# Optimization experiments

Measured on AMD Instinct MI355X. Metric: run time of the kernel, lower is better.

Reference implementation:

```python
import jax, jax.numpy as jnp
import numpy as np
import math

B, L, D, H = 4, 4096, 1024, 16
DH = D // H  # 64


def setup_inputs() -> dict:
    key = jax.random.key(0)
    ks = jax.random.split(key, 11)
    s = 1.0 / math.sqrt(D)
    return {
        "query": jax.random.normal(ks[0], (B, L, D), jnp.float32),
        "key_": jax.random.normal(ks[1], (B, L, D), jnp.float32),
        "value": jax.random.normal(ks[2], (B, L, D), jnp.float32),
        "Wq": jax.random.normal(ks[3], (D, D), jnp.float32) * s,
        "bq": jax.random.normal(ks[4], (D,), jnp.float32) * s,
        "Wk": jax.random.normal(ks[5], (D, D), jnp.float32) * s,
        "bk": jax.random.normal(ks[6], (D,), jnp.float32) * s,
        "Wv": jax.random.normal(ks[7], (D, D), jnp.float32) * s,
        "bv": jax.random.normal(ks[8], (D,), jnp.float32) * s,
        "Wo": jax.random.normal(ks[9], (D, D), jnp.float32) * s,
        "bo": jax.random.normal(ks[10], (D,), jnp.float32) * s,
    }


def reference(query, key_, value, Wq, bq, Wk, bk, Wv, bv, Wo, bo):
    # Linear projections (torch Linear: x @ W.T + b)
    q = (query @ Wq.T + bq).reshape(B, L, DH, H)   # heads in LAST dim (faithful quirk)
    k = (key_ @ Wk.T + bk).reshape(B, L, DH, H)
    v = (value @ Wv.T + bv).reshape(B, L, DH, H)
    # per-(batch, position) matmul: [B,L,DH,H] @ [B,L,H,DH] -> [B,L,DH,DH]
    scores = jnp.einsum('blih,bljh->blij', q, k) * jnp.asarray(math.sqrt(D), q.dtype)
    attn = jax.nn.softmax(scores, axis=-1)
    out = jnp.einsum('blij,bljh->blih', attn, v).reshape(B, L, D)
    return out @ Wo.T + bo
```

## Files before the change

### kernel.cpp

```cpp
#include <hip/hip_runtime.h>

typedef float    f32x4 __attribute__((ext_vector_type(4)));
typedef _Float16 h16x8 __attribute__((ext_vector_type(8)));
typedef _Float16 h16x4 __attribute__((ext_vector_type(4)));

#define DEV __device__ __forceinline__

DEV void async_load16(const void* g, void* l) {
  __builtin_amdgcn_global_load_lds((const __attribute__((address_space(1))) void*)g,
                                   (__attribute__((address_space(3))) void*)l,
                                   16, 0, 0);
}

template <bool OF32>
DEV void gemm256_core(const _Float16* __restrict__ A, const _Float16* __restrict__ Bw,
                      const float* __restrict__ bias, void* Cv, int bm, int bn) {
  constexpr int N = 1024;
  __shared__ __align__(16) _Float16 lds[2 * 2 * 2 * 8192];
  char* ldsb = (char*)lds;

  const int tid  = threadIdx.x;
  const int lane = tid & 63;
  const int w    = tid >> 6;
  const int wm   = w >> 2, wn = w & 3;
  const int m16  = lane & 15, q = lane >> 4;
  const int rowbase = bm << 8;
  const int colbase = bn << 8;

  const int sr0 = (w * 2 + 0) * 16 + (lane >> 2);
  const int sr1 = (w * 2 + 1) * 16 + (lane >> 2);
  const int ss  = lane & 3;
  const int sc0 = ((ss ^ ((sr0 ^ (sr0 >> 2)) & 3)) * 8);
  const int sc1 = ((ss ^ ((sr1 ^ (sr1 >> 2)) & 3)) * 8);

  auto stA = [&](int buf, int kk, int gk) {
    async_load16(A + (size_t)(rowbase + sr0) * 1024 + gk + kk * 32 + sc0,
                 ldsb + buf * 65536 + kk * 16384 + (w * 2 + 0) * 1024);
    async_load16(A + (size_t)(rowbase + sr1) * 1024 + gk + kk * 32 + sc1,
                 ldsb + buf * 65536 + kk * 16384 + (w * 2 + 1) * 1024);
  };
  auto stB = [&](int buf, int kk, int gk) {
    async_load16(Bw + (size_t)(colbase + sr0) * 1024 + gk + kk * 32 + sc0,
                 ldsb + buf * 65536 + 32768 + kk * 16384 + (w * 2 + 0) * 1024);
    async_load16(Bw + (size_t)(colbase + sr1) * 1024 + gk + kk * 32 + sc1,
                 ldsb + buf * 65536 + 32768 + kk * 16384 + (w * 2 + 1) * 1024);
  };

  int aoff[8], boff[4];
#pragma unroll
  for (int mt = 0; mt < 8; ++mt) {
    const int r = wm * 128 + mt * 16 + m16;
    aoff[mt] = r * 64 + ((q ^ ((r ^ (r >> 2)) & 3)) * 16);
  }
#pragma unroll
  for (int nt = 0; nt < 4; ++nt) {
    const int r = wn * 64 + nt * 16 + m16;
    boff[nt] = r * 64 + ((q ^ ((r ^ (r >> 2)) & 3)) * 16);
  }

  f32x4 acc[8][4];
#pragma unroll
  for (int nt = 0; nt < 4; ++nt) {
    const float bv = bias[colbase + wn * 64 + nt * 16 + m16];
#pragma unroll
    for (int mt = 0; mt < 8; ++mt) acc[mt][nt] = {bv, bv, bv, bv};
  }

  stA(0, 0, 0); stB(0, 0, 0); stA(0, 1, 0); stB(0, 1, 0);
  stA(1, 0, 64); stB(1, 0, 64);
  asm volatile("s_waitcnt vmcnt(4)" ::: "memory");
  __builtin_amdgcn_s_barrier();
  __builtin_amdgcn_sched_barrier(0);

  h16x8 bfr[4];

#define PHASE(BUF_, KK_, MH_, STAGE_, VM_)                                      \
  {                                                                             \
    const char* pA = ldsb + (BUF_) * 65536 + (KK_) * 16384;                     \
    const char* pB = pA + 32768;                                                \
    h16x8 a[4];                                                                 \
    _Pragma("unroll")                                                           \
    for (int m_ = 0; m_ < 4; ++m_)                                              \
      a[m_] = *(const h16x8*)(pA + aoff[(MH_) * 4 + m_]);                       \
    if ((MH_) == 0) {                                                           \
      _Pragma("unroll")                                                         \
      for (int n_ = 0; n_ < 4; ++n_)                                            \
        bfr[n_] = *(const h16x8*)(pB + boff[n_]);                               \
    }                                                                           \
    STAGE_                                                                      \
    VM_                                                                         \
    __builtin_amdgcn_s_barrier();                                               \
    asm volatile("s_waitcnt lgkmcnt(0)" ::: "memory");                          \
    __builtin_amdgcn_sched_barrier(0);                                          \
    __builtin_amdgcn_s_setprio(1);                                              \
    _Pragma("unroll")                                                           \
    for (int m_ = 0; m_ < 4; ++m_)                                              \
      _Pragma("unroll")                                                         \
      for (int n_ = 0; n_ < 4; ++n_)                                            \
        acc[(MH_) * 4 + m_][n_] = __builtin_amdgcn_mfma_f32_16x16x32_f16(       \
            a[m_], bfr[n_], acc[(MH_) * 4 + m_][n_], 0, 0, 0);                  \
    __builtin_amdgcn_s_setprio(0);                                              \
    __builtin_amdgcn_s_barrier();                                               \
    __builtin_amdgcn_sched_barrier(0);                                          \
  }

  for (int i = 0; i < 7; ++i) {
    const int g1 = (2 * i + 1) * 64, g2 = (2 * i + 2) * 64, g3 = (2 * i + 3) * 64;
    PHASE(0, 0, 0, { stA(1, 1, g1); stB(1, 1, g1); }, {})
    PHASE(0, 0, 1, {}, {})
    PHASE(0, 1, 0, { stA(0, 0, g2); }, {})
    PHASE(0, 1, 1, { stB(0, 0, g2); },
          { asm volatile("s_waitcnt vmcnt(4)" ::: "memory"); })
    PHASE(1, 0, 0, { stA(0, 1, g2); stB(0, 1, g2); }, {})
    PHASE(1, 0, 1, {}, {})
    PHASE(1, 1, 0, { stA(1, 0, g3); }, {})
    PHASE(1, 1, 1, { stB(1, 0, g3); },
          { asm volatile("s_waitcnt vmcnt(4)" ::: "memory"); })
  }
  {
    const int g1 = 15 * 64;
    PHASE(0, 0, 0, { stA(1, 1, g1); stB(1, 1, g1); }, {})
    PHASE(0, 0, 1, {}, {})
    PHASE(0, 1, 0, {}, {})
    PHASE(0, 1, 1, {}, { asm volatile("s_waitcnt vmcnt(0)" ::: "memory"); })
    PHASE(1, 0, 0, {}, {})
    PHASE(1, 0, 1, {}, {})
    PHASE(1, 1, 0, {}, {})
    PHASE(1, 1, 1, {}, {})
  }
#undef PHASE

#pragma unroll
  for (int mt = 0; mt < 8; ++mt) {
#pragma unroll
    for (int nt = 0; nt < 4; ++nt) {
      const int col = colbase + wn * 64 + nt * 16 + m16;
#pragma unroll
      for (int r = 0; r < 4; ++r) {
        const int row = rowbase + wm * 128 + mt * 16 + q * 4 + r;
        if constexpr (OF32)
          ((float*)Cv)[(size_t)row * N + col] = acc[mt][nt][r];
        else
          ((_Float16*)Cv)[(size_t)row * N + col] = (_Float16)acc[mt][nt][r];
      }
    }
  }
}

template <int AMODE, bool OF32>
DEV void gemm_core(const void* Av, const _Float16* __restrict__ Bw,
                   const float* __restrict__ bias, void* Cv) {
  constexpr int K = 1024, N = 1024;
  __shared__ __align__(16) _Float16 As[128 * 32];
  __shared__ __align__(16) _Float16 Bs[128 * 32];

  const int tid  = threadIdx.x;
  const int lane = tid & 63;
  const int w    = tid >> 6;
  const int d    = blockIdx.x;
  const int bm   = (d & 7) | ((d >> 6) << 3);
  const int bn   = (d >> 3) & 7;
  const int rowbase = bm << 7;
  const int colbase = bn << 7;
  const int wm = w >> 1, wn = w & 1;
  const int m16 = lane & 15, q = lane >> 4;
  const int brow = lane >> 2;
  const int bcol = (lane & 3) * 8;

  f32x4 acc[4][4];
#pragma unroll
  for (int nt = 0; nt < 4; ++nt) {
    const float bv = bias[colbase + wn * 64 + nt * 16 + m16];
#pragma unroll
    for (int mt = 0; mt < 4; ++mt) acc[mt][nt] = {bv, bv, bv, bv};
  }

  for (int ki = 0; ki < 32; ++ki) {
    const int k0 = ki * 32;
    if constexpr (AMODE == 0) {
      const _Float16* A = (const _Float16*)Av;
#pragma unroll
      for (int t = 0; t < 2; ++t)
        async_load16(A + (size_t)(rowbase + (w * 2 + t) * 16 + brow) * K + k0 + bcol,
                     &As[(w * 2 + t) * 512]);
    } else {
      const float* A = (const float*)Av;
#pragma unroll
      for (int i = 0; i < 4; ++i) {
        const int f = tid + i * 256;
        const int r = f >> 3, c4 = f & 7;
        const float4 v = *(const float4*)(A + (size_t)(rowbase + r) * K + k0 + c4 * 4);
        h16x4 o = {(_Float16)v.x, (_Float16)v.y, (_Float16)v.z, (_Float16)v.w};
        *(h16x4*)&As[r * 32 + c4 * 4] = o;
      }
    }
#pragma unroll
    for (int t = 0; t < 2; ++t)
      async_load16(Bw + (size_t)(colbase + (w * 2 + t) * 16 + brow) * K + k0 + bcol,
                   &Bs[(w * 2 + t) * 512]);
    __syncthreads();

    h16x8 af[4], bfr[4];
#pragma unroll
    for (int mt = 0; mt < 4; ++mt)
      af[mt] = *(const h16x8*)&As[(wm * 64 + mt * 16 + m16) * 32 + q * 8];
#pragma unroll
    for (int nt = 0; nt < 4; ++nt)
      bfr[nt] = *(const h16x8*)&Bs[(wn * 64 + nt * 16 + m16) * 32 + q * 8];
#pragma unroll
    for (int mt = 0; mt < 4; ++mt)
#pragma unroll
      for (int nt = 0; nt < 4; ++nt)
        acc[mt][nt] = __builtin_amdgcn_mfma_f32_16x16x32_f16(af[mt], bfr[nt], acc[mt][nt], 0, 0, 0);
    __syncthreads();
  }

#pragma unroll
  for (int mt = 0; mt < 4; ++mt) {
#pragma unroll
    for (int nt = 0; nt < 4; ++nt) {
      const int col = colbase + wn * 64 + nt * 16 + m16;
#pragma unroll
      for (int r = 0; r < 4; ++r) {
        const int row = rowbase + wm * 64 + mt * 16 + q * 4 + r;
        if constexpr (OF32)
          ((float*)Cv)[(size_t)row * N + col] = acc[mt][nt][r];
        else
          ((_Float16*)Cv)[(size_t)row * N + col] = (_Float16)acc[mt][nt][r];
      }
    }
  }
}

__global__ __launch_bounds__(256) void k_cvt_w(const float* __restrict__ Wq,
                                               const float* __restrict__ Wk,
                                               const float* __restrict__ Wv,
                                               const float* __restrict__ Wo,
                                               _Float16* __restrict__ dst) {
  const float* src;
  switch (blockIdx.y) {
    case 0: src = Wq; break;
    case 1: src = Wk; break;
    case 2: src = Wv; break;
    default: src = Wo; break;
  }
  _Float16* d = dst + (size_t)blockIdx.y * (1024 * 1024);
  const int idx = blockIdx.x * 256 + threadIdx.x;
  const float4 v = ((const float4*)src)[idx];
  h16x4 o = {(_Float16)v.x, (_Float16)v.y, (_Float16)v.z, (_Float16)v.w};
  ((h16x4*)d)[idx] = o;
}

__global__ __launch_bounds__(256) void k_cvt_a(const float* __restrict__ q,
                                               const float* __restrict__ k,
                                               const float* __restrict__ v,
                                               _Float16* __restrict__ dst) {
  const float* src = (blockIdx.y == 0) ? q : (blockIdx.y == 1) ? k : v;
  _Float16* d = dst + (size_t)blockIdx.y * ((size_t)16384 * 1024);
  const size_t idx = (size_t)blockIdx.x * 256 + threadIdx.x;
  const float4 vv = ((const float4*)src)[idx];
  h16x4 o = {(_Float16)vv.x, (_Float16)vv.y, (_Float16)vv.z, (_Float16)vv.w};
  ((h16x4*)d)[idx] = o;
}

__global__ __launch_bounds__(512, 2) void k_gemm_qkv_256(const _Float16* __restrict__ xf,
                                                         const _Float16* __restrict__ Wf,
                                                         const float* __restrict__ bq,
                                                         const float* __restrict__ bk,
                                                         const float* __restrict__ bv,
                                                         _Float16* __restrict__ proj) {
  constexpr size_t MW = 1024 * 1024, MA = (size_t)16384 * 1024;
  const int y = blockIdx.y;
  const float* bias = (y == 0) ? bq : (y == 1) ? bk : bv;
  const int d  = blockIdx.x;
  const int bm = (d & 7) + ((d >> 5) << 3);
  const int bn = (d >> 3) & 3;
  gemm256_core<false>(xf + y * MA, Wf + y * MW, bias, proj + y * MA, bm, bn);
}

__global__ __launch_bounds__(512, 2) void k_gemm_out_256(const _Float16* __restrict__ ao,
                                                         const _Float16* __restrict__ Wof,
                                                         const float* __restrict__ bo,
                                                         float* __restrict__ C) {
  const int d  = blockIdx.x;
  const int bm = (d & 7) + ((d >> 5) << 3);
  const int bn = (d >> 3) & 3;
  gemm256_core<true>(ao, Wof, bo, C, bm, bn);
}

__global__ __launch_bounds__(256) void k_gemm_qkv_f32(const float* __restrict__ q,
                                                      const float* __restrict__ k,
                                                      const float* __restrict__ v,
                                                      const _Float16* __restrict__ Wf,
                                                      const float* __restrict__ bq,
                                                      const float* __restrict__ bk,
                                                      const float* __restrict__ bv,
                                                      _Float16* __restrict__ proj) {
  constexpr size_t MW = 1024 * 1024, MA = (size_t)16384 * 1024;
  const int y = blockIdx.y;
  const float* A    = (y == 0) ? q  : (y == 1) ? k  : v;
  const float* bias = (y == 0) ? bq : (y == 1) ? bk : bv;
  gemm_core<1, false>(A, Wf + y * MW, bias, proj + y * MA);
}

__global__ __launch_bounds__(256) void k_attn(const _Float16* __restrict__ qp,
                                              const _Float16* __restrict__ kp,
                                              const _Float16* __restrict__ vp,
                                              _Float16* __restrict__ op) {
  constexpr int RS2 = 20;
  __shared__ __align__(16) _Float16 vsh[4][64 * RS2];
  const int w    = threadIdx.x >> 6;
  const int lane = threadIdx.x & 63;
  const int g    = lane >> 4;
  const int t    = lane & 15;
  const size_t base = ((size_t)blockIdx.x * 4 + w) * 1024;

  {
    h16x8 v0 = *(const h16x8*)(vp + base + lane * 16);
    h16x8 v1 = *(const h16x8*)(vp + base + lane * 16 + 8);
    _Float16* vr = &vsh[w][lane * RS2];
    h16x4 a0, a1, a2, a3;
#pragma unroll
    for (int e = 0; e < 4; ++e) {
      a0[e] = v0[e]; a1[e] = v0[4 + e]; a2[e] = v1[e]; a3[e] = v1[4 + e];
    }
    *(h16x4*)(vr + 0)  = a0;
    *(h16x4*)(vr + 4)  = a1;
    *(h16x4*)(vr + 8)  = a2;
    *(h16x4*)(vr + 12) = a3;
  }

  h16x4 kA[4], qB[4];
#pragma unroll
  for (int jt = 0; jt < 4; ++jt) {
    kA[jt] = *(const h16x4*)(kp + base + (jt * 16 + t) * 16 + g * 4);
    qB[jt] = *(const h16x4*)(qp + base + (jt * 16 + t) * 16 + g * 4);
  }

  f32x4 st[4][4];
#pragma unroll
  for (int jt = 0; jt < 4; ++jt)
#pragma unroll
    for (int nt = 0; nt < 4; ++nt)
      st[jt][nt] = __builtin_amdgcn_mfma_f32_16x16x16f16(
          kA[jt], qB[nt], (f32x4){0.f, 0.f, 0.f, 0.f}, 0, 0, 0);

  h16x4 pb[4][4];
  float inv[4];
#pragma unroll
  for (int nt = 0; nt < 4; ++nt) {
    float mx = -3.0e38f;
#pragma unroll
    for (int jt = 0; jt < 4; ++jt)
#pragma unroll
      for (int r = 0; r < 4; ++r) mx = fmaxf(mx, st[jt][nt][r]);
    mx = fmaxf(mx, __shfl_xor(mx, 16));
    mx = fmaxf(mx, __shfl_xor(mx, 32));
    float sum = 0.f;
#pragma unroll
    for (int jt = 0; jt < 4; ++jt) {
#pragma unroll
      for (int r = 0; r < 4; ++r) {
        const float p = __expf((st[jt][nt][r] - mx) * 32.0f);
        sum += p;
        pb[jt][nt][r] = (_Float16)p;
      }
    }
    sum += __shfl_xor(sum, 16);
    sum += __shfl_xor(sum, 32);
    inv[nt] = 1.0f / sum;
  }

  h16x4 vA[4];
#pragma unroll
  for (int kt = 0; kt < 4; ++kt)
#pragma unroll
    for (int e = 0; e < 4; ++e)
      vA[kt][e] = vsh[w][(kt * 16 + g * 4 + e) * RS2 + t];

#pragma unroll
  for (int it = 0; it < 4; ++it) {
    f32x4 ot = {0.f, 0.f, 0.f, 0.f};
#pragma unroll
    for (int kt = 0; kt < 4; ++kt)
      ot = __builtin_amdgcn_mfma_f32_16x16x16f16(vA[kt], pb[kt][it], ot, 0, 0, 0);
    h16x4 o;
#pragma unroll
    for (int r = 0; r < 4; ++r) o[r] = (_Float16)(ot[r] * inv[it]);
    *(h16x4*)(op + base + (it * 16 + t) * 16 + g * 4) = o;
  }
}

extern "C" void kernel_launch(void* const* d_in, const int* in_sizes, int n_in,
                              void* d_out, int out_size, void* d_ws, size_t ws_size,
                              hipStream_t stream) {
  const float* query = (const float*)d_in[0];
  const float* key_  = (const float*)d_in[1];
  const float* value = (const float*)d_in[2];
  const float* Wq    = (const float*)d_in[3];
  const float* bq    = (const float*)d_in[4];
  const float* Wk    = (const float*)d_in[5];
  const float* bk    = (const float*)d_in[6];
  const float* Wv    = (const float*)d_in[7];
  const float* bv    = (const float*)d_in[8];
  const float* Wo    = (const float*)d_in[9];
  const float* bo    = (const float*)d_in[10];

  constexpr size_t MW = 1024 * 1024;
  constexpr size_t MA = (size_t)16384 * 1024;

  _Float16* Wf = (_Float16*)d_ws;
  const size_t needA = (4 * MW + 6 * MA) * sizeof(_Float16);

  k_cvt_w<<<dim3(1024, 4), 256, 0, stream>>>(Wq, Wk, Wv, Wo, Wf);

  if (ws_size >= needA) {
    _Float16* xf   = Wf + 4 * MW;
    _Float16* proj = xf + 3 * MA;
    _Float16* ao   = xf;
    k_cvt_a<<<dim3(16384, 3), 256, 0, stream>>>(query, key_, value, xf);
    k_gemm_qkv_256<<<dim3(256, 3), 512, 0, stream>>>(xf, Wf, bq, bk, bv, proj);
    k_attn<<<4096, 256, 0, stream>>>(proj, proj + MA, proj + 2 * MA, ao);
    k_gemm_out_256<<<256, 512, 0, stream>>>(ao, Wf + 3 * MW, bo, (float*)d_out);
  } else {
    _Float16* proj = Wf + 4 * MW;
    _Float16* ao   = proj + 3 * MA;
    k_gemm_qkv_f32<<<dim3(1024, 3), 256, 0, stream>>>(query, key_, value, Wf,
                                                      bq, bk, bv, proj);
    k_attn<<<4096, 256, 0, stream>>>(proj, proj + MA, proj + 2 * MA, ao);
    k_gemm_out_256<<<256, 512, 0, stream>>>(ao, Wf + 3 * MW, bo, (float*)d_out);
  }
}
```

Measured before the change: 419.8 us.

## Fuse fp32-to-fp16 activation conversion into 256-tile QKV GEMM loads

Removes the separate activation conversion kernel and instead has the 256x256 QKV GEMM load fp32 activations into registers, convert them to fp16 and write them into swizzled LDS, while weights still stream in via async global-to-LDS loads. This eliminates writing and rereading three 32 MB fp16 activation copies. The cost is a more complex software pipeline with manual waitcnt accounting and doubled global read bytes for A inside the GEMM, plus register pressure from the staging buffers.

```diff
diff --git a/kernel.cpp b/kernel.cpp
--- a/kernel.cpp
+++ b/kernel.cpp
@@ -5,11 +5,174 @@
 typedef _Float16 h16x4 __attribute__((ext_vector_type(4)));
 
 #define DEV __device__ __forceinline__
+#define VMW(N) asm volatile("s_waitcnt vmcnt(" #N ")" ::: "memory")
 
 DEV void async_load16(const void* g, void* l) {
   __builtin_amdgcn_global_load_lds((const __attribute__((address_space(1))) void*)g,
                                    (__attribute__((address_space(3))) void*)l,
                                    16, 0, 0);
+}
+
+
+__global__ __launch_bounds__(512, 2) void k_gemm_qkv_f32_256(
+    const float* __restrict__ q, const float* __restrict__ k,
+    const float* __restrict__ v, const _Float16* __restrict__ Wf,
+    const float* __restrict__ bq, const float* __restrict__ bk,
+    const float* __restrict__ bv, _Float16* __restrict__ proj) {
+  constexpr size_t MW = 1024 * 1024, MA = (size_t)16384 * 1024;
+  const int y = blockIdx.y;
+  const float* __restrict__ A    = (y == 0) ? q  : (y == 1) ? k  : v;
+  const float* __restrict__ bias = (y == 0) ? bq : (y == 1) ? bk : bv;
+  const _Float16* __restrict__ Bw = Wf + y * MW;
+  _Float16* __restrict__ C = proj + y * MA;
+
+  __shared__ __align__(16) _Float16 lds[2 * 2 * 2 * 8192];
+  char* ldsb = (char*)lds;
+
+  const int tid  = threadIdx.x;
+  const int lane = tid & 63;
+  const int w    = tid >> 6;
+  const int wm   = w >> 2, wn = w & 3;
+  const int m16  = lane & 15, qq = lane >> 4;
+  const int d    = blockIdx.x;
+  const int bm   = (d & 7) + ((d >> 5) << 3);
+  const int bn   = (d >> 3) & 3;
+  const int rowbase = bm << 8;
+  const int colbase = bn << 8;
+
+  const int rr  = lane >> 2, ss = lane & 3;
+  const int xsw = (rr ^ (rr >> 2)) & 3;
+  const int sc  = (ss ^ xsw) * 8;
+
+  const size_t ar0 = (size_t)(rowbase + (w * 2 + 0) * 16 + rr) * 1024 + ss * 8;
+  const size_t ar1 = (size_t)(rowbase + (w * 2 + 1) * 16 + rr) * 1024 + ss * 8;
+  const size_t br0 = (size_t)(colbase + (w * 2 + 0) * 16 + rr) * 1024 + sc;
+  const size_t br1 = (size_t)(colbase + (w * 2 + 1) * 16 + rr) * 1024 + sc;
+  const int adst0 = (w * 2 + 0) * 1024 + rr * 64 + (ss ^ xsw) * 16;
+  const int adst1 = (w * 2 + 1) * 1024 + rr * 64 + (ss ^ xsw) * 16;
+
+  auto stBone = [&](int buf, int kk, int gk) {
+    async_load16(Bw + br0 + gk + kk * 32,
+                 ldsb + buf * 65536 + 32768 + kk * 16384 + (w * 2 + 0) * 1024);
+    async_load16(Bw + br1 + gk + kk * 32,
+                 ldsb + buf * 65536 + 32768 + kk * 16384 + (w * 2 + 1) * 1024);
+  };
+
+  f32x4 ra[4], rb[4];
+  auto aload = [&](f32x4* r, int gkf) {
+    r[0] = *(const f32x4*)(A + ar0 + gkf);
+    r[1] = *(const f32x4*)(A + ar0 + gkf + 4);
+    r[2] = *(const f32x4*)(A + ar1 + gkf);
+    r[3] = *(const f32x4*)(A + ar1 + gkf + 4);
+  };
+  auto awrite = [&](const f32x4* r, int buf, int kk) {
+    h16x8 o0, o1;
+#pragma unroll
+    for (int e = 0; e < 4; ++e) {
+      o0[e]     = (_Float16)r[0][e];
+      o0[4 + e] = (_Float16)r[1][e];
+      o1[e]     = (_Float16)r[2][e];
+      o1[4 + e] = (_Float16)r[3][e];
+    }
+    *(h16x8*)(ldsb + buf * 65536 + kk * 16384 + adst0) = o0;
+    *(h16x8*)(ldsb + buf * 65536 + kk * 16384 + adst1) = o1;
+  };
+
+  int aoff[8], boff[4];
+#pragma unroll
+  for (int mt = 0; mt < 8; ++mt) {
+    const int r = wm * 128 + mt * 16 + m16;
+    aoff[mt] = r * 64 + ((qq ^ ((r ^ (r >> 2)) & 3)) * 16);
+  }
+#pragma unroll
+  for (int nt = 0; nt < 4; ++nt) {
+    const int r = wn * 64 + nt * 16 + m16;
+    boff[nt] = r * 64 + ((qq ^ ((r ^ (r >> 2)) & 3)) * 16);
+  }
+
+  f32x4 acc[8][4];
+#pragma unroll
+  for (int nt = 0; nt < 4; ++nt) {
+    const float bv = bias[colbase + wn * 64 + nt * 16 + m16];
+#pragma unroll
+    for (int mt = 0; mt < 8; ++mt) acc[mt][nt] = {bv, bv, bv, bv};
+  }
+
+  aload(ra, 0); aload(rb, 32);
+  awrite(ra, 0, 0);
+  awrite(rb, 0, 1);
+  stBone(0, 0, 0); stBone(0, 1, 0);
+  aload(ra, 64); stBone(1, 0, 64);
+  aload(rb, 96); stBone(1, 1, 64);
+  VMW(8);
+  asm volatile("s_waitcnt lgkmcnt(0)" ::: "memory");
+  __builtin_amdgcn_sched_barrier(0);
+  __builtin_amdgcn_s_barrier();
+
+  h16x8 bfr[4];
+
+#define PH(BUF_, KK_, MH_, STAGE_)                                              \
+  {                                                                             \
+    const char* pA = ldsb + (BUF_) * 65536 + (KK_) * 16384;                     \
+    const char* pB = pA + 32768;                                                \
+    h16x8 a[4];                                                                 \
+    _Pragma("unroll")                                                           \
+    for (int m_ = 0; m_ < 4; ++m_)                                              \
+      a[m_] = *(const h16x8*)(pA + aoff[(MH_) * 4 + m_]);                       \
+    if ((MH_) == 0) {                                                           \
+      _Pragma("unroll")                                                         \
+      for (int n_ = 0; n_ < 4; ++n_)                                            \
+        bfr[n_] = *(const h16x8*)(pB + boff[n_]);                               \
+    }                                                                           \
+    STAGE_                                                                      \
+    asm volatile("s_waitcnt lgkmcnt(0)" ::: "memory");                          \
+    __builtin_amdgcn_sched_barrier(0);                                          \
+    __builtin_amdgcn_s_barrier();                                               \
+    __builtin_amdgcn_s_setprio(1);                                              \
+    _Pragma("unroll")                                                           \
+    for (int m_ = 0; m_ < 4; ++m_)                                              \
+      _Pragma("unroll")                                                         \
+      for (int n_ = 0; n_ < 4; ++n_)                                            \
+        acc[(MH_) * 4 + m_][n_] = __builtin_amdgcn_mfma_f32_16x16x32_f16(       \
+            a[m_], bfr[n_], acc[(MH_) * 4 + m_][n_], 0, 0, 0);                  \
+    __builtin_amdgcn_s_setprio(0);                                              \
+    __builtin_amdgcn_s_barrier();                                               \
+    __builtin_amdgcn_sched_barrier(0);                                          \
+  }
+
+  for (int i = 0; i < 7; ++i) {
+    const int gA0 = (2 * i + 2) * 64, gA1 = (2 * i + 3) * 64;
+    PH(0, 0, 0, { VMW(8); awrite(ra, 1, 0); })
+    PH(0, 0, 1, { VMW(2); awrite(rb, 1, 1); })
+    PH(0, 1, 0, { aload(ra, gA0); })
+    PH(0, 1, 1, { aload(rb, gA0 + 32); VMW(8); })
+    PH(1, 0, 0, { awrite(ra, 0, 0); stBone(0, 0, gA0); })
+    PH(1, 0, 1, { awrite(rb, 0, 1); stBone(0, 1, gA0); })
+    PH(1, 1, 0, { aload(ra, gA1); stBone(1, 0, gA1); })
+    PH(1, 1, 1, { aload(rb, gA1 + 32); stBone(1, 1, gA1); VMW(12); })
+  }
+  PH(0, 0, 0, { VMW(8); awrite(ra, 1, 0); })
+  PH(0, 0, 1, { VMW(2); awrite(rb, 1, 1); })
+  PH(0, 1, 0, {})
+  PH(0, 1, 1, { VMW(0); })
+  PH(1, 0, 0, {})
+  PH(1, 0, 1, {})
+  PH(1, 1, 0, {})
+  PH(1, 1, 1, {})
+#undef PH
+
+#pragma unroll
+  for (int mt = 0; mt < 8; ++mt) {
+#pragma unroll
+    for (int nt = 0; nt < 4; ++nt) {
+      const int col = colbase + wn * 64 + nt * 16 + m16;
+#pragma unroll
+      for (int r = 0; r < 4; ++r) {
+        const int row = rowbase + wm * 128 + mt * 16 + qq * 4 + r;
+        C[(size_t)row * 1024 + col] = (_Float16)acc[mt][nt][r];
+      }
+    }
+  }
 }
 
 template <bool OF32>
@@ -251,33 +414,6 @@
   ((h16x4*)d)[idx] = o;
 }
 
-__global__ __launch_bounds__(256) void k_cvt_a(const float* __restrict__ q,
-                                               const float* __restrict__ k,
-                                               const float* __restrict__ v,
-                                               _Float16* __restrict__ dst) {
-  const float* src = (blockIdx.y == 0) ? q : (blockIdx.y == 1) ? k : v;
-  _Float16* d = dst + (size_t)blockIdx.y * ((size_t)16384 * 1024);
-  const size_t idx = (size_t)blockIdx.x * 256 + threadIdx.x;
-  const float4 vv = ((const float4*)src)[idx];
-  h16x4 o = {(_Float16)vv.x, (_Float16)vv.y, (_Float16)vv.z, (_Float16)vv.w};
-  ((h16x4*)d)[idx] = o;
-}
-
-__global__ __launch_bounds__(512, 2) void k_gemm_qkv_256(const _Float16* __restrict__ xf,
-                                                         const _Float16* __restrict__ Wf,
-                                                         const float* __restrict__ bq,
-                                                         const float* __restrict__ bk,
-                                                         const float* __restrict__ bv,
-                                                         _Float16* __restrict__ proj) {
-  constexpr size_t MW = 1024 * 1024, MA = (size_t)16384 * 1024;
-  const int y = blockIdx.y;
-  const float* bias = (y == 0) ? bq : (y == 1) ? bk : bv;
-  const int d  = blockIdx.x;
-  const int bm = (d & 7) + ((d >> 5) << 3);
-  const int bn = (d >> 3) & 3;
-  gemm256_core<false>(xf + y * MA, Wf + y * MW, bias, proj + y * MA, bm, bn);
-}
-
 __global__ __launch_bounds__(512, 2) void k_gemm_out_256(const _Float16* __restrict__ ao,
                                                          const _Float16* __restrict__ Wof,
                                                          const float* __restrict__ bo,
@@ -288,14 +424,11 @@
   gemm256_core<true>(ao, Wof, bo, C, bm, bn);
 }
 
-__global__ __launch_bounds__(256) void k_gemm_qkv_f32(const float* __restrict__ q,
-                                                      const float* __restrict__ k,
-                                                      const float* __restrict__ v,
-                                                      const _Float16* __restrict__ Wf,
-                                                      const float* __restrict__ bq,
-                                                      const float* __restrict__ bk,
-                                                      const float* __restrict__ bv,
-                                                      _Float16* __restrict__ proj) {
+__global__ __launch_bounds__(256) void k_gemm_qkv_f32_legacy(
+    const float* __restrict__ q, const float* __restrict__ k,
+    const float* __restrict__ v, const _Float16* __restrict__ Wf,
+    const float* __restrict__ bq, const float* __restrict__ bk,
+    const float* __restrict__ bv, _Float16* __restrict__ proj) {
   constexpr size_t MW = 1024 * 1024, MA = (size_t)16384 * 1024;
   const int y = blockIdx.y;
   const float* A    = (y == 0) ? q  : (y == 1) ? k  : v;
@@ -409,24 +542,21 @@
   constexpr size_t MW = 1024 * 1024;
   constexpr size_t MA = (size_t)16384 * 1024;
 
-  _Float16* Wf = (_Float16*)d_ws;
-  const size_t needA = (4 * MW + 6 * MA) * sizeof(_Float16);
+  _Float16* Wf   = (_Float16*)d_ws;
+  _Float16* proj = Wf + 4 * MW;
+  _Float16* ao   = proj + 3 * MA;
+  const size_t need = (4 * MW + 4 * MA) * sizeof(_Float16);
 
   k_cvt_w<<<dim3(1024, 4), 256, 0, stream>>>(Wq, Wk, Wv, Wo, Wf);
 
-  if (ws_size >= needA) {
-    _Float16* xf   = Wf + 4 * MW;
-    _Float16* proj = xf + 3 * MA;
-    _Float16* ao   = xf;
-    k_cvt_a<<<dim3(16384, 3), 256, 0, stream>>>(query, key_, value, xf);
-    k_gemm_qkv_256<<<dim3(256, 3), 512, 0, stream>>>(xf, Wf, bq, bk, bv, proj);
+  if (ws_size >= need) {
+    k_gemm_qkv_f32_256<<<dim3(256, 3), 512, 0, stream>>>(query, key_, value, Wf,
+                                                         bq, bk, bv, proj);
     k_attn<<<4096, 256, 0, stream>>>(proj, proj + MA, proj + 2 * MA, ao);
     k_gemm_out_256<<<256, 512, 0, stream>>>(ao, Wf + 3 * MW, bo, (float*)d_out);
   } else {
-    _Float16* proj = Wf + 4 * MW;
-    _Float16* ao   = proj + 3 * MA;
-    k_gemm_qkv_f32<<<dim3(1024, 3), 256, 0, stream>>>(query, key_, value, Wf,
-                                                      bq, bk, bv, proj);
+    k_gemm_qkv_f32_legacy<<<dim3(1024, 3), 256, 0, stream>>>(query, key_, value, Wf,
+                                                             bq, bk, bv, proj);
     k_attn<<<4096, 256, 0, stream>>>(proj, proj + MA, proj + 2 * MA, ao);
     k_gemm_out_256<<<256, 512, 0, stream>>>(ao, Wf + 3 * MW, bo, (float*)d_out);
   }
```

Result: slower. 505.3 us (+20.4%).

## Merge conversion kernels and stage attention Q/K/output through LDS for coalescing

Applied to the files above, without the earlier changes.

Combines the weight and activation fp16 conversion kernels into a single launch to remove one kernel launch and its tail. In the per-position attention kernel, Q and K are now loaded with wide coalesced 16-byte reads and staged through padded shared memory, replacing strided 8-byte global loads. The output is likewise written to shared memory first and stored with wide coalesced writes. The cost is extra LDS traffic and a larger shared-memory footprint, which may lower occupancy.

```diff
diff --git a/kernel.cpp b/kernel.cpp
--- a/kernel.cpp
+++ b/kernel.cpp
@@ -232,6 +232,32 @@
   }
 }
 
+__global__ __launch_bounds__(256) void k_cvt_all(const float* __restrict__ Wq,
+                                                 const float* __restrict__ Wk,
+                                                 const float* __restrict__ Wv,
+                                                 const float* __restrict__ Wo,
+                                                 const float* __restrict__ q,
+                                                 const float* __restrict__ k,
+                                                 const float* __restrict__ v,
+                                                 _Float16* __restrict__ dst) {
+  const size_t i4 = (size_t)blockIdx.x * 256 + threadIdx.x;
+  const float* src;
+  size_t off;
+  if (i4 < (1u << 20)) {
+    const int wi = (int)(i4 >> 18);
+    src = (wi == 0) ? Wq : (wi == 1) ? Wk : (wi == 2) ? Wv : Wo;
+    off = i4 & ((1u << 18) - 1);
+  } else {
+    const size_t j = i4 - (1u << 20);
+    const int ai = (int)(j >> 22);
+    src = (ai == 0) ? q : (ai == 1) ? k : v;
+    off = j & ((1u << 22) - 1);
+  }
+  const float4 vv = ((const float4*)src)[off];
+  h16x4 o = {(_Float16)vv.x, (_Float16)vv.y, (_Float16)vv.z, (_Float16)vv.w};
+  ((h16x4*)dst)[i4] = o;
+}
+
 __global__ __launch_bounds__(256) void k_cvt_w(const float* __restrict__ Wq,
                                                const float* __restrict__ Wk,
                                                const float* __restrict__ Wv,
@@ -248,18 +274,6 @@
   const int idx = blockIdx.x * 256 + threadIdx.x;
   const float4 v = ((const float4*)src)[idx];
   h16x4 o = {(_Float16)v.x, (_Float16)v.y, (_Float16)v.z, (_Float16)v.w};
-  ((h16x4*)d)[idx] = o;
-}
-
-__global__ __launch_bounds__(256) void k_cvt_a(const float* __restrict__ q,
-                                               const float* __restrict__ k,
-                                               const float* __restrict__ v,
-                                               _Float16* __restrict__ dst) {
-  const float* src = (blockIdx.y == 0) ? q : (blockIdx.y == 1) ? k : v;
-  _Float16* d = dst + (size_t)blockIdx.y * ((size_t)16384 * 1024);
-  const size_t idx = (size_t)blockIdx.x * 256 + threadIdx.x;
-  const float4 vv = ((const float4*)src)[idx];
-  h16x4 o = {(_Float16)vv.x, (_Float16)vv.y, (_Float16)vv.z, (_Float16)vv.w};
   ((h16x4*)d)[idx] = o;
 }
 
@@ -288,14 +302,11 @@
   gemm256_core<true>(ao, Wof, bo, C, bm, bn);
 }
 
-__global__ __launch_bounds__(256) void k_gemm_qkv_f32(const float* __restrict__ q,
-                                                      const float* __restrict__ k,
-                                                      const float* __restrict__ v,
-                                                      const _Float16* __restrict__ Wf,
-                                                      const float* __restrict__ bq,
-                                                      const float* __restrict__ bk,
-                                                      const float* __restrict__ bv,
-                                                      _Float16* __restrict__ proj) {
+__global__ __launch_bounds__(256) void k_gemm_qkv_f32_legacy(
+    const float* __restrict__ q, const float* __restrict__ k,
+    const float* __restrict__ v, const _Float16* __restrict__ Wf,
+    const float* __restrict__ bq, const float* __restrict__ bk,
+    const float* __restrict__ bv, _Float16* __restrict__ proj) {
   constexpr size_t MW = 1024 * 1024, MA = (size_t)16384 * 1024;
   const int y = blockIdx.y;
   const float* A    = (y == 0) ? q  : (y == 1) ? k  : v;
@@ -307,8 +318,10 @@
                                               const _Float16* __restrict__ kp,
                                               const _Float16* __restrict__ vp,
                                               _Float16* __restrict__ op) {
-  constexpr int RS2 = 20;
-  __shared__ __align__(16) _Float16 vsh[4][64 * RS2];
+  constexpr int RS = 20;
+  __shared__ __align__(16) _Float16 qsh[4][64 * RS];
+  __shared__ __align__(16) _Float16 ksh[4][64 * RS];
+  __shared__ __align__(16) _Float16 vsh[4][64 * RS];
   const int w    = threadIdx.x >> 6;
   const int lane = threadIdx.x & 63;
   const int g    = lane >> 4;
@@ -316,25 +329,44 @@
   const size_t base = ((size_t)blockIdx.x * 4 + w) * 1024;
 
   {
+    h16x8 q0 = *(const h16x8*)(qp + base + lane * 16);
+    h16x8 q1 = *(const h16x8*)(qp + base + lane * 16 + 8);
+    h16x8 k0 = *(const h16x8*)(kp + base + lane * 16);
+    h16x8 k1 = *(const h16x8*)(kp + base + lane * 16 + 8);
     h16x8 v0 = *(const h16x8*)(vp + base + lane * 16);
     h16x8 v1 = *(const h16x8*)(vp + base + lane * 16 + 8);
-    _Float16* vr = &vsh[w][lane * RS2];
-    h16x4 a0, a1, a2, a3;
-#pragma unroll
-    for (int e = 0; e < 4; ++e) {
-      a0[e] = v0[e]; a1[e] = v0[4 + e]; a2[e] = v1[e]; a3[e] = v1[4 + e];
-    }
-    *(h16x4*)(vr + 0)  = a0;
-    *(h16x4*)(vr + 4)  = a1;
-    *(h16x4*)(vr + 8)  = a2;
-    *(h16x4*)(vr + 12) = a3;
+    _Float16* qr = &qsh[w][lane * RS];
+    _Float16* kr = &ksh[w][lane * RS];
+    _Float16* vr = &vsh[w][lane * RS];
+#pragma unroll
+    for (int c = 0; c < 2; ++c) {
+      h16x4 a;
+#pragma unroll
+      for (int e = 0; e < 4; ++e) a[e] = q0[c * 4 + e];
+      *(h16x4*)(qr + c * 4) = a;
+#pragma unroll
+      for (int e = 0; e < 4; ++e) a[e] = q1[c * 4 + e];
+      *(h16x4*)(qr + 8 + c * 4) = a;
+#pragma unroll
+      for (int e = 0; e < 4; ++e) a[e] = k0[c * 4 + e];
+      *(h16x4*)(kr + c * 4) = a;
+#pragma unroll
+      for (int e = 0; e < 4; ++e) a[e] = k1[c * 4 + e];
+      *(h16x4*)(kr + 8 + c * 4) = a;
+#pragma unroll
+      for (int e = 0; e < 4; ++e) a[e] = v0[c * 4 + e];
+      *(h16x4*)(vr + c * 4) = a;
+#pragma unroll
+      for (int e = 0; e < 4; ++e) a[e] = v1[c * 4 + e];
+      *(h16x4*)(vr + 8 + c * 4) = a;
+    }
   }
 
   h16x4 kA[4], qB[4];
 #pragma unroll
   for (int jt = 0; jt < 4; ++jt) {
-    kA[jt] = *(const h16x4*)(kp + base + (jt * 16 + t) * 16 + g * 4);
-    qB[jt] = *(const h16x4*)(qp + base + (jt * 16 + t) * 16 + g * 4);
+    kA[jt] = *(const h16x4*)&ksh[w][(jt * 16 + t) * RS + g * 4];
+    qB[jt] = *(const h16x4*)&qsh[w][(jt * 16 + t) * RS + g * 4];
   }
 
   f32x4 st[4][4];
@@ -376,7 +408,7 @@
   for (int kt = 0; kt < 4; ++kt)
 #pragma unroll
     for (int e = 0; e < 4; ++e)
-      vA[kt][e] = vsh[w][(kt * 16 + g * 4 + e) * RS2 + t];
+      vA[kt][e] = vsh[w][(kt * 16 + g * 4 + e) * RS + t];
 
 #pragma unroll
   for (int it = 0; it < 4; ++it) {
@@ -387,7 +419,22 @@
     h16x4 o;
 #pragma unroll
     for (int r = 0; r < 4; ++r) o[r] = (_Float16)(ot[r] * inv[it]);
-    *(h16x4*)(op + base + (it * 16 + t) * 16 + g * 4) = o;
+    *(h16x4*)&qsh[w][(it * 16 + t) * RS + g * 4] = o;
+  }
+  {
+    const _Float16* orow = &qsh[w][lane * RS];
+    h16x4 o0 = *(const h16x4*)(orow + 0);
+    h16x4 o1 = *(const h16x4*)(orow + 4);
+    h16x4 o2 = *(const h16x4*)(orow + 8);
+    h16x4 o3 = *(const h16x4*)(orow + 12);
+    h16x8 w0, w1;
+#pragma unroll
+    for (int e = 0; e < 4; ++e) {
+      w0[e] = o0[e]; w0[4 + e] = o1[e];
+      w1[e] = o2[e]; w1[4 + e] = o3[e];
+    }
+    *(h16x8*)(op + base + lane * 16) = w0;
+    *(h16x8*)(op + base + lane * 16 + 8) = w1;
   }
 }
 
@@ -412,21 +459,20 @@
   _Float16* Wf = (_Float16*)d_ws;
   const size_t needA = (4 * MW + 6 * MA) * sizeof(_Float16);
 
-  k_cvt_w<<<dim3(1024, 4), 256, 0, stream>>>(Wq, Wk, Wv, Wo, Wf);
-
   if (ws_size >= needA) {
     _Float16* xf   = Wf + 4 * MW;
     _Float16* proj = xf + 3 * MA;
     _Float16* ao   = xf;
-    k_cvt_a<<<dim3(16384, 3), 256, 0, stream>>>(query, key_, value, xf);
+    k_cvt_all<<<53248, 256, 0, stream>>>(Wq, Wk, Wv, Wo, query, key_, value, Wf);
     k_gemm_qkv_256<<<dim3(256, 3), 512, 0, stream>>>(xf, Wf, bq, bk, bv, proj);
     k_attn<<<4096, 256, 0, stream>>>(proj, proj + MA, proj + 2 * MA, ao);
     k_gemm_out_256<<<256, 512, 0, stream>>>(ao, Wf + 3 * MW, bo, (float*)d_out);
   } else {
     _Float16* proj = Wf + 4 * MW;
     _Float16* ao   = proj + 3 * MA;
-    k_gemm_qkv_f32<<<dim3(1024, 3), 256, 0, stream>>>(query, key_, value, Wf,
-                                                      bq, bk, bv, proj);
+    k_cvt_w<<<dim3(1024, 4), 256, 0, stream>>>(Wq, Wk, Wv, Wo, Wf);
+    k_gemm_qkv_f32_legacy<<<dim3(1024, 3), 256, 0, stream>>>(query, key_, value, Wf,
+                                                             bq, bk, bv, proj);
     k_attn<<<4096, 256, 0, stream>>>(proj, proj + MA, proj + 2 * MA, ao);
     k_gemm_out_256<<<256, 512, 0, stream>>>(ao, Wf + 3 * MW, bo, (float*)d_out);
   }
```

Measured after the change: 414.3 us. No clear change (-1.3%).
